# Performance work log

Hardware: AMD Instinct MI355X
Metric: run time of the kernel (lower is better)

Reference implementation:

```python
import jax, jax.numpy as jnp
import numpy as np

# Involution2D config (matches init_kwargs)
F = 256          # filters
K = 3            # kernel_size
G = 16           # groups
RR = 4           # reduce_ratio
BN_EPS = 1e-3    # keras BatchNormalization default epsilon


def setup_inputs() -> dict:
    key = jax.random.key(0)
    ks = jax.random.split(key, 8)
    C = 256
    Cr = F // RR                    # reduce_mapping channels = 64
    KKG = K * K * G                 # span_mapping channels = 144
    s = lambda k, sh, fan: jax.random.normal(k, sh, jnp.float32) * (1.0 / np.sqrt(fan))
    return {
        "x": jax.random.normal(ks[0], (4, 128, 128, C), jnp.float32),
        # reduce_mapping: 1x1 conv + BN(inference) + relu
        "Wr": s(ks[1], (C, Cr), C),
        "br": jnp.zeros((Cr,), jnp.float32),
        "gamma": jnp.ones((Cr,), jnp.float32),
        "beta": jnp.zeros((Cr,), jnp.float32),
        "mean": jax.random.normal(ks[2], (Cr,), jnp.float32) * 0.1,
        "var": jax.random.uniform(ks[3], (Cr,), jnp.float32, 0.5, 1.5),
        # span_mapping: 1x1 conv -> K*K*G dynamic weights
        "Ws": s(ks[4], (Cr, KKG), Cr),
        "bs": jnp.zeros((KKG,), jnp.float32),
        # initial_mapping: 1x1 conv -> F (applied since F != K*K*G)
        "Wi": s(ks[5], (C, F), C),
        "bi": jnp.zeros((F,), jnp.float32),
    }


def reference(x, Wr, br, gamma, beta, mean, var, Ws, bs, Wi, bi):
    B, H, W, _ = x.shape
    KK = K * K
    # reduce_mapping: 1x1 conv + BN(inference) + relu
    r = jnp.einsum('bhwc,cd->bhwd', x, Wr) + br
    r = jax.nn.relu((r - mean) * jax.lax.rsqrt(var + BN_EPS) * gamma + beta)
    # span_mapping: per-pixel dynamic kernel weights [B,H,W,KK*G] -> [B,H,W,G,1,KK]
    w = jnp.einsum('bhwd,dk->bhwk', r, Ws) + bs
    w = w.reshape(B, H, W, G, KK)[:, :, :, :, None, :]
    # initial_mapping: 1x1 conv -> F channels
    xi = jnp.einsum('bhwc,cf->bhwf', x, Wi) + bi
    # tf.image.extract_patches (SAME, stride=1, rate=1): layout is
    # (kernel_pos major, channel minor), i.e. flat index = kpos*F + c
    pad = (K - 1) // 2
    xp = jnp.pad(xi, ((0, 0), (pad, pad), (pad, pad), (0, 0)))
    patches = jnp.stack(
        [xp[:, i:i + H, j:j + W, :] for i in range(K) for j in range(K)],
        axis=3)                                   # [B,H,W,KK,F]
    # faithful to the original K.reshape of the flat [KK*F] axis
    patches = patches.reshape(B, H, W, G, F // G, KK)
    out = jnp.sum(w * patches, axis=-1)           # [B,H,W,G,F//G]
    return out.reshape(B, H, W, F)
```

## Files before the change

### kernel.cpp

```cpp
#include <hip/hip_runtime.h>

#define BN_EPS 1e-3f

typedef __attribute__((ext_vector_type(8))) short bf16x8;
typedef __attribute__((ext_vector_type(4))) float f32x4;

__device__ inline unsigned short f2b(float f) {
    unsigned int u = __float_as_uint(f);
    unsigned int r = (u + 0x7fffu + ((u >> 16) & 1u)) >> 16;
    return (unsigned short)r;
}
__device__ inline float b2f(unsigned short h) {
    return __uint_as_float(((unsigned int)h) << 16);
}
__device__ inline unsigned int pk2(float a, float b) {
    unsigned int r;
    asm("v_cvt_pk_bf16_f32 %0, %1, %2" : "=v"(r) : "v"(a), "v"(b));
    return r;
}
__device__ inline float dot2bf(unsigned int x, unsigned int w, float acc) {
    float r;
    asm("v_dot2_f32_bf16 %0, %1, %2, %3" : "=v"(r) : "v"(x), "v"(w), "v"(acc));
    return r;
}

__global__ void k_prep(const float* __restrict__ Wi, const float* __restrict__ Wr,
                       const float* __restrict__ Ws,
                       unsigned short* __restrict__ Bt, unsigned short* __restrict__ Wst) {
    int t = blockIdx.x * 256 + threadIdx.x;
    if (t < 320 * 256) {
        int n = t >> 8, k = t & 255;
        float v = (n < 256) ? Wi[k * 256 + n] : Wr[k * 64 + (n - 256)];
        Bt[t] = f2b(v);
    } else {
        int t2 = t - 320 * 256;
        if (t2 < 144 * 64) {
            int n = t2 >> 6, k = t2 & 63;
            Wst[t2] = f2b(Ws[k * 144 + n]);
        }
    }
}

__device__ __forceinline__ void gather8(const int* dwp, const unsigned* pkA,
                                        const unsigned* pkB, float w0f, float w8f,
                                        float* res) {
#pragma unroll
    for (int ff = 0; ff < 8; ++ff) {
        const int e0 = ff * 9;
        float a;
        if ((ff & 1) == 0) {
            const int d0 = e0 >> 1;
            a = __uint_as_float(((unsigned)dwp[d0 + 4]) << 16) * w8f;
            a = dot2bf((unsigned)dwp[d0 + 0], pkA[0], a);
            a = dot2bf((unsigned)dwp[d0 + 1], pkA[1], a);
            a = dot2bf((unsigned)dwp[d0 + 2], pkA[2], a);
            a = dot2bf((unsigned)dwp[d0 + 3], pkA[3], a);
        } else {
            const int di = e0 >> 1;
            const int d1 = di + 1;
            a = __uint_as_float(((unsigned)dwp[di]) & 0xffff0000u) * w0f;
            a = dot2bf((unsigned)dwp[d1 + 0], pkB[0], a);
            a = dot2bf((unsigned)dwp[d1 + 1], pkB[1], a);
            a = dot2bf((unsigned)dwp[d1 + 2], pkB[2], a);
            a = dot2bf((unsigned)dwp[d1 + 3], pkB[3], a);
        }
        res[ff] = a;
    }
}

#define XIP 264
#define RS_OFF (180 * XIP)
#define RSP 72
#define WL_OFF (RS_OFF + 180 * RSP)
#define SMN (WL_OFF + 128 * 144)

__global__ __launch_bounds__(512, 2) void k_fused(
    const float* __restrict__ x, const unsigned short* __restrict__ Bt,
    const unsigned short* __restrict__ Wst,
    const float* __restrict__ bi, const float* __restrict__ br,
    const float* __restrict__ gamma, const float* __restrict__ beta,
    const float* __restrict__ mean, const float* __restrict__ var,
    const float* __restrict__ bs, float* __restrict__ out)
{
    __shared__ __attribute__((aligned(16))) unsigned short sm[SMN];
    const int tid = threadIdx.x;
    const int bx = blockIdx.x;
    const int w0 = (bx & 7) * 16;
    const int h0 = ((bx >> 3) & 15) * 8;
    const int bb = bx >> 7;

    const int wv = tid >> 6;
    const int lane = tid & 63;
    const int col = lane & 15;
    const int quad = lane >> 4;

    const float bi_v0 = bi[(2 * wv) * 16 + col];
    const float bi_v1 = bi[(2 * wv + 1) * 16 + col];
    const int dcl = (wv & 3) * 16 + col;
    const float brd = br[dcl];
    const float md  = mean[dcl];
    const float sc  = gamma[dcl] * rsqrtf(var[dcl] + BN_EPS);
    const float btv = beta[dcl];

    bf16x8 bx0[8], bx1[8], brr[8];
    {
        const unsigned short* p0 = &Bt[((2 * wv) * 16 + col) * 256];
        const unsigned short* p1 = &Bt[((2 * wv + 1) * 16 + col) * 256];
#pragma unroll
        for (int kc = 0; kc < 8; ++kc) {
            bx0[kc] = *(const bf16x8*)&p0[kc * 32 + quad * 8];
            bx1[kc] = *(const bf16x8*)&p1[kc * 32 + quad * 8];
        }
        if (wv < 4) {
            const unsigned short* pr = &Bt[((16 + wv) * 16 + col) * 256];
#pragma unroll
            for (int kc = 0; kc < 8; ++kc)
                brr[kc] = *(const bf16x8*)&pr[kc * 32 + quad * 8];
        }
    }

    const int chq = (tid & 15) * 4;

#pragma unroll
    for (int pc = 0; pc < 2; ++pc) {
        float4 vcur[4];
        const int hp = pc * 32 + (tid >> 4);
        int r = hp / 18, cc = hp - r * 18;
        int gh = h0 - 1 + r, gw = w0 - 1 + cc;
        bool ok = ((unsigned)gh < 128u) && ((unsigned)gw < 128u);
        if (ok) {
            const float* src = x + (((long long)(bb * 128 + gh)) * 128 + gw) * 256 + chq;
#pragma unroll
            for (int j = 0; j < 4; ++j) vcur[j] = *(const float4*)&src[j * 64];
        } else {
#pragma unroll
            for (int j = 0; j < 4; ++j) vcur[j] = (float4){0.f, 0.f, 0.f, 0.f};
        }
#pragma unroll
        for (int j = 0; j < 4; ++j) {
            uint2 pk;
            pk.x = pk2(vcur[j].x, vcur[j].y);
            pk.y = pk2(vcur[j].z, vcur[j].w);
            *(uint2*)&sm[hp * XIP + chq + j * 64] = pk;
        }
    }
    __syncthreads();

    bf16x8 aA0[8], aA1[8];
    {
        const int rowA0 = col * XIP;
        const int rowA1 = (16 + col) * XIP;
#pragma unroll
        for (int kc = 0; kc < 8; ++kc) {
            const int kb = kc * 32 + quad * 8;
            aA0[kc] = *(const bf16x8*)&sm[rowA0 + kb];
            aA1[kc] = *(const bf16x8*)&sm[rowA1 + kb];
        }
    }

    for (int c = 0; c < 6; ++c) {
        float4 vn[4];
        int hp_n = 200;
        if (c < 4) {
            hp_n = (c + 2) * 32 + (tid >> 4);
            int r = hp_n / 18, cc = hp_n - r * 18;
            int gh = h0 - 1 + r, gw = w0 - 1 + cc;
            bool ok = (hp_n < 180) && ((unsigned)gh < 128u) && ((unsigned)gw < 128u);
            if (ok) {
                const float* src = x + (((long long)(bb * 128 + gh)) * 128 + gw) * 256 + chq;
#pragma unroll
                for (int j = 0; j < 4; ++j) vn[j] = *(const float4*)&src[j * 64];
            } else {
#pragma unroll
                for (int j = 0; j < 4; ++j) vn[j] = (float4){0.f, 0.f, 0.f, 0.f};
            }
        }

        f32x4 a00 = {0.f,0.f,0.f,0.f}, a01 = a00, a10 = a00, a11 = a00;
        f32x4 ar0 = a00, ar1 = a00;
#pragma unroll
        for (int kc = 0; kc < 8; ++kc) {
            a00 = __builtin_amdgcn_mfma_f32_16x16x32_bf16(aA0[kc], bx0[kc], a00, 0, 0, 0);
            a10 = __builtin_amdgcn_mfma_f32_16x16x32_bf16(aA1[kc], bx0[kc], a10, 0, 0, 0);
            a01 = __builtin_amdgcn_mfma_f32_16x16x32_bf16(aA0[kc], bx1[kc], a01, 0, 0, 0);
            a11 = __builtin_amdgcn_mfma_f32_16x16x32_bf16(aA1[kc], bx1[kc], a11, 0, 0, 0);
            if (wv < 4) {
                ar0 = __builtin_amdgcn_mfma_f32_16x16x32_bf16(aA0[kc], brr[kc], ar0, 0, 0, 0);
                ar1 = __builtin_amdgcn_mfma_f32_16x16x32_bf16(aA1[kc], brr[kc], ar1, 0, 0, 0);
            }
        }
        __syncthreads();

        if (c < 5) {
            const int rowA0 = ((c + 1) * 32 + col) * XIP;
            const int rowA1 = ((c + 1) * 32 + 16 + col) * XIP;
#pragma unroll
            for (int kc = 0; kc < 8; ++kc) {
                const int kb = kc * 32 + quad * 8;
                aA0[kc] = *(const bf16x8*)&sm[rowA0 + kb];
                aA1[kc] = *(const bf16x8*)&sm[rowA1 + kb];
            }
        }

        {
            const int n0 = (2 * wv) * 16 + col;
            const int n1 = (2 * wv + 1) * 16 + col;
            const int rb = c * 32 + quad * 4;
#pragma unroll
            for (int rg = 0; rg < 4; ++rg) {
                const int r0 = rb + rg, r1 = rb + 16 + rg;
                if (r0 < 180) {
                    const unsigned int u0 = pk2(a00[rg] + bi_v0, a01[rg] + bi_v1);
                    sm[r0 * XIP + n0] = (unsigned short)u0;
                    sm[r0 * XIP + n1] = (unsigned short)(u0 >> 16);
                }
                if (r1 < 180) {
                    const unsigned int u1 = pk2(a10[rg] + bi_v0, a11[rg] + bi_v1);
                    sm[r1 * XIP + n0] = (unsigned short)u1;
                    sm[r1 * XIP + n1] = (unsigned short)(u1 >> 16);
                }
            }
            if (wv < 4) {
#pragma unroll
                for (int rg = 0; rg < 4; ++rg) {
                    const int r0 = rb + rg, r1 = rb + 16 + rg;
                    if (r0 < 180) {
                        float v = (ar0[rg] + brd - md) * sc + btv;
                        sm[RS_OFF + r0 * RSP + dcl] = f2b(fmaxf(v, 0.f));
                    }
                    if (r1 < 180) {
                        float v = (ar1[rg] + brd - md) * sc + btv;
                        sm[RS_OFF + r1 * RSP + dcl] = f2b(fmaxf(v, 0.f));
                    }
                }
            }
        }

        if (c < 4 && hp_n < 180) {
#pragma unroll
            for (int j = 0; j < 4; ++j) {
                uint2 pk;
                pk.x = pk2(vn[j].x, vn[j].y);
                pk.y = pk2(vn[j].z, vn[j].w);
                *(uint2*)&sm[hp_n * XIP + chq + j * 64] = pk;
            }
        }
    }
    __syncthreads();

    {
        f32x4 wacc[9];
#pragma unroll
        for (int j = 0; j < 9; ++j) wacc[j] = (f32x4){0.f, 0.f, 0.f, 0.f};
        const int arow = (19 + wv * 18 + col) * RSP;
#pragma unroll
        for (int kc = 0; kc < 2; ++kc) {
            const int kb = kc * 32 + quad * 8;
            bf16x8 ra = *(const bf16x8*)&sm[RS_OFF + arow + kb];
#pragma unroll
            for (int j = 0; j < 9; ++j) {
                bf16x8 wb = *(const bf16x8*)&Wst[(j * 16 + col) * 64 + kb];
                wacc[j] = __builtin_amdgcn_mfma_f32_16x16x32_bf16(ra, wb, wacc[j], 0, 0, 0);
            }
        }
        const int prow = wv * 16 + quad * 4;
#pragma unroll
        for (int j = 0; j < 8; j += 2) {
            const int na = j * 16 + col;
            const int nb = na + 16;
            const float bva = bs[na];
            const float bvb = bs[nb];
#pragma unroll
            for (int rg = 0; rg < 4; ++rg) {
                const unsigned int u = pk2(wacc[j][rg] + bva, wacc[j + 1][rg] + bvb);
                sm[WL_OFF + (prow + rg) * 144 + na] = (unsigned short)u;
                sm[WL_OFF + (prow + rg) * 144 + nb] = (unsigned short)(u >> 16);
            }
        }
        {
            const int n = 8 * 16 + col;
            const float bv = bs[n];
#pragma unroll
            for (int rg = 0; rg < 4; ++rg)
                sm[WL_OFF + (prow + rg) * 144 + n] = f2b(wacc[8][rg] + bv);
        }
    }
    __syncthreads();

    {
        const int g = tid & 15;
        const int pb = tid >> 4;

        const int idx0 = g * 144;
        const int kp0  = idx0 >> 8;
        const int c0   = idx0 & 255;
        int len1 = 256 - c0; if (len1 > 144) len1 = 144;
        const int kp1  = kp0 + 1;
        const int koff0 = (kp0 / 3) * 18 + (kp0 % 3);
        const int koff1 = (kp1 <= 8) ? ((kp1 / 3) * 18 + (kp1 % 3)) : 0;

#pragma unroll
        for (int jj = 0; jj < 4; ++jj) {
            const int p = pb + 32 * jj;
            const int phb = (p >> 4) * 18 + (p & 15);
            const int base0 = (phb + koff0) * XIP + c0;
            const int base1 = (phb + koff1) * XIP;

            unsigned wsv[9];
#pragma unroll
            for (int kk = 0; kk < 9; ++kk)
                wsv[kk] = sm[WL_OFF + p * 144 + g * 9 + kk];
            unsigned pkA[4], pkB[4];
#pragma unroll
            for (int k = 0; k < 4; ++k) {
                pkA[k] = (wsv[2 * k + 1] << 16) | wsv[2 * k];
                pkB[k] = (wsv[2 * k + 2] << 16) | wsv[2 * k + 1];
            }
            const float w0f = __uint_as_float(wsv[0] << 16);
            const float w8f = __uint_as_float(wsv[8] << 16);

            float res[16];
            {
                int4 xv[9];
#pragma unroll
                for (int i = 0; i < 9; ++i) {
                    const int e = i * 8;
                    const int addr = (e < len1) ? (base0 + e) : (base1 + (e - len1));
                    xv[i] = *(const int4*)&sm[addr];
                }
                gather8((const int*)xv, pkA, pkB, w0f, w8f, res);
            }
            {
                int4 xv[9];
#pragma unroll
                for (int i = 9; i < 18; ++i) {
                    const int e = i * 8;
                    const int addr = (e < len1) ? (base0 + e) : (base1 + (e - len1));
                    xv[i - 9] = *(const int4*)&sm[addr];
                }
                gather8((const int*)xv, pkA, pkB, w0f, w8f, res + 8);
            }

            const long long orow =
                (((long long)(bb * 128 + h0 + (p >> 4))) * 128 + (w0 + (p & 15))) * 256 + g * 16;
#pragma unroll
            for (int q = 0; q < 4; ++q) {
                float4 o = {res[q * 4 + 0], res[q * 4 + 1], res[q * 4 + 2], res[q * 4 + 3]};
                *(float4*)&out[orow + q * 4] = o;
            }
        }
    }
}

extern "C" void kernel_launch(void* const* d_in, const int* in_sizes, int n_in,
                              void* d_out, int out_size, void* d_ws, size_t ws_size,
                              hipStream_t stream) {
    const float* x     = (const float*)d_in[0];
    const float* Wr    = (const float*)d_in[1];
    const float* br    = (const float*)d_in[2];
    const float* gamma = (const float*)d_in[3];
    const float* beta  = (const float*)d_in[4];
    const float* mean  = (const float*)d_in[5];
    const float* var   = (const float*)d_in[6];
    const float* Ws    = (const float*)d_in[7];
    const float* bs    = (const float*)d_in[8];
    const float* Wi    = (const float*)d_in[9];
    const float* bi    = (const float*)d_in[10];
    float* out = (float*)d_out;

    unsigned char* ws = (unsigned char*)d_ws;
    unsigned short* Bt  = (unsigned short*)(ws + 0);
    unsigned short* Wst = (unsigned short*)(ws + 163840);

    k_prep<<<dim3(356), dim3(256), 0, stream>>>(Wi, Wr, Ws, Bt, Wst);
    k_fused<<<dim3(512), dim3(512), 0, stream>>>(
        x, Bt, Wst, bi, br, gamma, beta, mean, var, bs, out);
}
```

Before: 172.4 us.

## Double-buffer MFMA accumulators and prefetch x two chunks ahead

Restructures the per-chunk loop of the fused 1x1-conv stage. The MFMA work for chunk c+1 is issued before chunk c's results are written back to shared memory, using ping-pong accumulator sets. The global x prefetch now runs two chunks ahead, also ping-ponged. A-operands are read from LDS straight into the MFMAs instead of being staged in 16 register vectors. The goal is to hide epilogue stores and global-load latency behind matrix work, at the cost of a second accumulator set and prefetch buffer that raise register pressure.

Result: no change. 172.2 us (-0.1%).

```diff
diff --git a/kernel.cpp b/kernel.cpp
--- a/kernel.cpp
+++ b/kernel.cpp
@@ -144,61 +144,96 @@
             *(uint2*)&sm[hp * XIP + chq + j * 64] = pk;
         }
     }
+
+    float4 vnP[4], vnQ[4];
+    int hpP = 200, hpQ = 200;
+    {
+        hpP = 2 * 32 + (tid >> 4);
+        int r = hpP / 18, cc = hpP - r * 18;
+        int gh = h0 - 1 + r, gw = w0 - 1 + cc;
+        bool ok = (hpP < 180) && ((unsigned)gh < 128u) && ((unsigned)gw < 128u);
+        if (ok) {
+            const float* src = x + (((long long)(bb * 128 + gh)) * 128 + gw) * 256 + chq;
+#pragma unroll
+            for (int j = 0; j < 4; ++j) vnP[j] = *(const float4*)&src[j * 64];
+        } else {
+#pragma unroll
+            for (int j = 0; j < 4; ++j) vnP[j] = (float4){0.f, 0.f, 0.f, 0.f};
+        }
+    }
     __syncthreads();
 
-    bf16x8 aA0[8], aA1[8];
+    f32x4 accP[6], accQ[6];
+#pragma unroll
+    for (int j = 0; j < 6; ++j) {
+        accP[j] = (f32x4){0.f, 0.f, 0.f, 0.f};
+        accQ[j] = accP[j];
+    }
+
     {
         const int rowA0 = col * XIP;
         const int rowA1 = (16 + col) * XIP;
 #pragma unroll
         for (int kc = 0; kc < 8; ++kc) {
             const int kb = kc * 32 + quad * 8;
-            aA0[kc] = *(const bf16x8*)&sm[rowA0 + kb];
-            aA1[kc] = *(const bf16x8*)&sm[rowA1 + kb];
-        }
-    }
-
+            bf16x8 a0 = *(const bf16x8*)&sm[rowA0 + kb];
+            bf16x8 a1 = *(const bf16x8*)&sm[rowA1 + kb];
+            accP[0] = __builtin_amdgcn_mfma_f32_16x16x32_bf16(a0, bx0[kc], accP[0], 0, 0, 0);
+            accP[1] = __builtin_amdgcn_mfma_f32_16x16x32_bf16(a0, bx1[kc], accP[1], 0, 0, 0);
+            accP[2] = __builtin_amdgcn_mfma_f32_16x16x32_bf16(a1, bx0[kc], accP[2], 0, 0, 0);
+            accP[3] = __builtin_amdgcn_mfma_f32_16x16x32_bf16(a1, bx1[kc], accP[3], 0, 0, 0);
+            if (wv < 4) {
+                accP[4] = __builtin_amdgcn_mfma_f32_16x16x32_bf16(a0, brr[kc], accP[4], 0, 0, 0);
+                accP[5] = __builtin_amdgcn_mfma_f32_16x16x32_bf16(a1, brr[kc], accP[5], 0, 0, 0);
+            }
+        }
+    }
+
+#pragma unroll
     for (int c = 0; c < 6; ++c) {
-        float4 vn[4];
-        int hp_n = 200;
-        if (c < 4) {
-            hp_n = (c + 2) * 32 + (tid >> 4);
-            int r = hp_n / 18, cc = hp_n - r * 18;
-            int gh = h0 - 1 + r, gw = w0 - 1 + cc;
-            bool ok = (hp_n < 180) && ((unsigned)gh < 128u) && ((unsigned)gw < 128u);
+        f32x4* A  = (c & 1) ? accQ : accP;
+        f32x4* B  = (c & 1) ? accP : accQ;
+        float4* vS = (c & 1) ? vnQ : vnP;
+        float4* vI = (c & 1) ? vnP : vnQ;
+        const int hpS = (c & 1) ? hpQ : hpP;
+
+        __syncthreads();
+
+        int hpI = 200;
+        if (c < 3) {
+            hpI = (c + 3) * 32 + (tid >> 4);
+            int r = hpI / 18, cc2 = hpI - r * 18;
+            int gh = h0 - 1 + r, gw = w0 - 1 + cc2;
+            bool ok = (hpI < 180) && ((unsigned)gh < 128u) && ((unsigned)gw < 128u);
             if (ok) {
                 const float* src = x + (((long long)(bb * 128 + gh)) * 128 + gw) * 256 + chq;
 #pragma unroll
-                for (int j = 0; j < 4; ++j) vn[j] = *(const float4*)&src[j * 64];
+                for (int j = 0; j < 4; ++j) vI[j] = *(const float4*)&src[j * 64];
             } else {
 #pragma unroll
-                for (int j = 0; j < 4; ++j) vn[j] = (float4){0.f, 0.f, 0.f, 0.f};
-            }
-        }
-
-        f32x4 a00 = {0.f,0.f,0.f,0.f}, a01 = a00, a10 = a00, a11 = a00;
-        f32x4 ar0 = a00, ar1 = a00;
-#pragma unroll
-        for (int kc = 0; kc < 8; ++kc) {
-            a00 = __builtin_amdgcn_mfma_f32_16x16x32_bf16(aA0[kc], bx0[kc], a00, 0, 0, 0);
-            a10 = __builtin_amdgcn_mfma_f32_16x16x32_bf16(aA1[kc], bx0[kc], a10, 0, 0, 0);
-            a01 = __builtin_amdgcn_mfma_f32_16x16x32_bf16(aA0[kc], bx1[kc], a01, 0, 0, 0);
-            a11 = __builtin_amdgcn_mfma_f32_16x16x32_bf16(aA1[kc], bx1[kc], a11, 0, 0, 0);
-            if (wv < 4) {
-                ar0 = __builtin_amdgcn_mfma_f32_16x16x32_bf16(aA0[kc], brr[kc], ar0, 0, 0, 0);
-                ar1 = __builtin_amdgcn_mfma_f32_16x16x32_bf16(aA1[kc], brr[kc], ar1, 0, 0, 0);
-            }
-        }
-        __syncthreads();
+                for (int j = 0; j < 4; ++j) vI[j] = (float4){0.f, 0.f, 0.f, 0.f};
+            }
+        }
+        if (c & 1) hpP = hpI; else hpQ = hpI;
 
         if (c < 5) {
+#pragma unroll
+            for (int j = 0; j < 6; ++j) B[j] = (f32x4){0.f, 0.f, 0.f, 0.f};
             const int rowA0 = ((c + 1) * 32 + col) * XIP;
-            const int rowA1 = ((c + 1) * 32 + 16 + col) * XIP;
+            const int rowA1 = rowA0 + 16 * XIP;
 #pragma unroll
             for (int kc = 0; kc < 8; ++kc) {
                 const int kb = kc * 32 + quad * 8;
-                aA0[kc] = *(const bf16x8*)&sm[rowA0 + kb];
-                aA1[kc] = *(const bf16x8*)&sm[rowA1 + kb];
+                bf16x8 a0 = *(const bf16x8*)&sm[rowA0 + kb];
+                bf16x8 a1 = *(const bf16x8*)&sm[rowA1 + kb];
+                B[0] = __builtin_amdgcn_mfma_f32_16x16x32_bf16(a0, bx0[kc], B[0], 0, 0, 0);
+                B[1] = __builtin_amdgcn_mfma_f32_16x16x32_bf16(a0, bx1[kc], B[1], 0, 0, 0);
+                B[2] = __builtin_amdgcn_mfma_f32_16x16x32_bf16(a1, bx0[kc], B[2], 0, 0, 0);
+                B[3] = __builtin_amdgcn_mfma_f32_16x16x32_bf16(a1, bx1[kc], B[3], 0, 0, 0);
+                if (wv < 4) {
+                    B[4] = __builtin_amdgcn_mfma_f32_16x16x32_bf16(a0, brr[kc], B[4], 0, 0, 0);
+                    B[5] = __builtin_amdgcn_mfma_f32_16x16x32_bf16(a1, brr[kc], B[5], 0, 0, 0);
+                }
             }
         }
 
@@ -210,12 +245,12 @@
             for (int rg = 0; rg < 4; ++rg) {
                 const int r0 = rb + rg, r1 = rb + 16 + rg;
                 if (r0 < 180) {
-                    const unsigned int u0 = pk2(a00[rg] + bi_v0, a01[rg] + bi_v1);
+                    const unsigned int u0 = pk2(A[0][rg] + bi_v0, A[1][rg] + bi_v1);
                     sm[r0 * XIP + n0] = (unsigned short)u0;
                     sm[r0 * XIP + n1] = (unsigned short)(u0 >> 16);
                 }
                 if (r1 < 180) {
-                    const unsigned int u1 = pk2(a10[rg] + bi_v0, a11[rg] + bi_v1);
+                    const unsigned int u1 = pk2(A[2][rg] + bi_v0, A[3][rg] + bi_v1);
                     sm[r1 * XIP + n0] = (unsigned short)u1;
                     sm[r1 * XIP + n1] = (unsigned short)(u1 >> 16);
                 }
@@ -225,24 +260,24 @@
                 for (int rg = 0; rg < 4; ++rg) {
                     const int r0 = rb + rg, r1 = rb + 16 + rg;
                     if (r0 < 180) {
-                        float v = (ar0[rg] + brd - md) * sc + btv;
+                        float v = (A[4][rg] + brd - md) * sc + btv;
                         sm[RS_OFF + r0 * RSP + dcl] = f2b(fmaxf(v, 0.f));
                     }
                     if (r1 < 180) {
-                        float v = (ar1[rg] + brd - md) * sc + btv;
+                        float v = (A[5][rg] + brd - md) * sc + btv;
                         sm[RS_OFF + r1 * RSP + dcl] = f2b(fmaxf(v, 0.f));
                     }
                 }
             }
         }
 
-        if (c < 4 && hp_n < 180) {
+        if (c < 4 && hpS < 180) {
 #pragma unroll
             for (int j = 0; j < 4; ++j) {
                 uint2 pk;
-                pk.x = pk2(vn[j].x, vn[j].y);
-                pk.y = pk2(vn[j].z, vn[j].w);
-                *(uint2*)&sm[hp_n * XIP + chq + j * 64] = pk;
+                pk.x = pk2(vS[j].x, vS[j].y);
+                pk.y = pk2(vS[j].z, vS[j].w);
+                *(uint2*)&sm[hpS * XIP + chq + j * 64] = pk;
             }
         }
     }
```
